# Performance work log

Measured on AMD Instinct MI355X. Metric: run time of the kernel, lower is better.

Reference implementation:

```python
import jax, jax.numpy as jnp
import numpy as np

EPS = 1e-5

def layer_norm(x, g, b):
    m = x.mean(-1, keepdims=True)
    v = ((x - m) ** 2).mean(-1, keepdims=True)
    return (x - m) * jax.lax.rsqrt(v + EPS) * g + b

def setup_inputs() -> dict:
    key = jax.random.key(0)
    ks = jax.random.split(key, 12)
    H = 2048; E = 2048; I = 2048; N = 32
    A = (H + E) // 2  # attention hidden = 2048
    s = lambda fan: 1.0 / np.sqrt(fan)
    inp = {
        "input":   jax.random.normal(ks[0], (I,), jnp.float32),
        "hiddens": jax.random.normal(ks[1], (N, H), jnp.float32),
        "cells":   jax.random.normal(ks[2], (N, H), jnp.float32),
        "external":jax.random.normal(ks[3], (E,), jnp.float32),
        # weights (torch nn.Linear layout: [out, in]); LN enabled -> no biases on linears
        "W_ai":   jax.random.uniform(ks[4], (A, H + E), jnp.float32, -s(H+E), s(H+E)),
        "W_attn": jax.random.uniform(ks[5], (1, A), jnp.float32, -s(A), s(A)),
        "W_merge":jax.random.uniform(ks[6], (H, H), jnp.float32, -s(H), s(H)),
        "W_iou":  jax.random.uniform(ks[7], (3 * H, I + H), jnp.float32, -s(I+H), s(I+H)),
        "W_fi":   jax.random.uniform(ks[8], (H, I), jnp.float32, -s(I), s(I)),
        "W_fh":   jax.random.uniform(ks[9], (H, H), jnp.float32, -s(H), s(H)),
        "g_merge": jnp.ones((H,), jnp.float32), "b_merge": jnp.zeros((H,), jnp.float32),
        "g_f": jnp.ones((H,), jnp.float32), "b_f": jnp.zeros((H,), jnp.float32),
        "g_i": jnp.ones((H,), jnp.float32), "b_i": jnp.zeros((H,), jnp.float32),
        "g_o": jnp.ones((H,), jnp.float32), "b_o": jnp.zeros((H,), jnp.float32),
        "g_u": jnp.ones((H,), jnp.float32), "b_u": jnp.zeros((H,), jnp.float32),
        "g_c": jnp.ones((H,), jnp.float32), "b_c": jnp.zeros((H,), jnp.float32),
    }
    return inp

def reference(input, hiddens, cells, external,
              W_ai, W_attn, W_merge, W_iou, W_fi, W_fh,
              g_merge, b_merge, g_f, b_f, g_i, b_i, g_o, b_o, g_u, b_u, g_c, b_c):
    N, H = hiddens.shape
    # forget-gate preactivations: [H] + [N,H] -> [N,H]
    f_lin = input @ W_fi.T + hiddens @ W_fh.T
    # attentive merge over children
    ext = jnp.broadcast_to(external, (N, external.shape[0]))
    ai = jnp.tanh(jnp.concatenate([hiddens, ext], axis=1) @ W_ai.T)       # [N, (H+E)//2]
    attn = jax.nn.softmax(ai @ W_attn.T, axis=0)                          # [N, 1]
    merged = (hiddens * attn).sum(0)                                      # [H]
    merge_hidden = jnp.tanh(layer_norm(merged @ W_merge.T, g_merge, b_merge))
    # i/o/u gates from [input ; merged_hidden]
    iou = jnp.concatenate([input, merge_hidden]) @ W_iou.T                # [3H]
    i_l, o_l, u_l = jnp.split(iou, 3)
    f = jax.nn.sigmoid(layer_norm(f_lin, g_f, b_f))                       # [N,H]
    i = jax.nn.sigmoid(layer_norm(i_l, g_i, b_i))
    o = jax.nn.sigmoid(layer_norm(o_l, g_o, b_o))
    u = jnp.tanh(layer_norm(u_l, g_u, b_u))                               # dropout=0 -> identity
    new_cell = layer_norm(i * u + (f * cells).sum(0), g_c, b_c)           # [H]
    new_h = o * jnp.tanh(new_cell)
    return new_h, new_cell
```

## Files before the change

### kernel.cpp

```cpp
#include <hip/hip_runtime.h>
#include <hip/hip_bf16.h>

typedef __bf16 bf16_t;
typedef __attribute__((ext_vector_type(8))) __bf16 bf16x8;
typedef __attribute__((ext_vector_type(4))) float f32x4;

#define EPSF 1e-5f

__global__ __launch_bounds__(256) void gemm32_mfma(
    const float* __restrict__ Hd, const float* __restrict__ W,
    float* __restrict__ C, int M, int K, int wstride, int jtiles)
{
    int bx   = blockIdx.x;
    int jt   = bx % jtiles;
    int nt   = bx / jtiles;
    int tid  = threadIdx.x;
    int wave = tid >> 6;
    int lane = tid & 63;
    int l15  = lane & 15;
    int quad = lane >> 4;
    int kper = K >> 2;
    int k0   = wave * kper;

    const float* ap = Hd + (size_t)(nt * 16 + l15) * 2048 + quad * 8 + k0;
    const float* bp = W  + (size_t)(jt * 16 + l15) * wstride + quad * 8 + k0;

    f32x4 acc = {0.f, 0.f, 0.f, 0.f};
    for (int k = 0; k < kper; k += 32) {
        float4 a0 = *(const float4*)(ap + k);
        float4 a1 = *(const float4*)(ap + k + 4);
        float4 b0 = *(const float4*)(bp + k);
        float4 b1 = *(const float4*)(bp + k + 4);
        bf16x8 av, bv;
        av[0] = (bf16_t)a0.x; av[1] = (bf16_t)a0.y; av[2] = (bf16_t)a0.z; av[3] = (bf16_t)a0.w;
        av[4] = (bf16_t)a1.x; av[5] = (bf16_t)a1.y; av[6] = (bf16_t)a1.z; av[7] = (bf16_t)a1.w;
        bv[0] = (bf16_t)b0.x; bv[1] = (bf16_t)b0.y; bv[2] = (bf16_t)b0.z; bv[3] = (bf16_t)b0.w;
        bv[4] = (bf16_t)b1.x; bv[5] = (bf16_t)b1.y; bv[6] = (bf16_t)b1.z; bv[7] = (bf16_t)b1.w;
        acc = __builtin_amdgcn_mfma_f32_16x16x32_bf16(av, bv, acc, 0, 0, 0);
    }

    __shared__ float red[4][16][16];
    #pragma unroll
    for (int r = 0; r < 4; ++r) red[wave][quad * 4 + r][l15] = acc[r];
    __syncthreads();

    int row = tid >> 4, col = tid & 15;
    float s = red[0][row][col] + red[1][row][col] + red[2][row][col] + red[3][row][col];
    C[(size_t)(nt * 16 + row) * M + jt * 16 + col] = s;
}

__global__ __launch_bounds__(256) void gemv_k(
    const float* __restrict__ W, const float* __restrict__ x,
    float* __restrict__ out, int K, int wstride)
{
    int row  = blockIdx.x * 4 + (threadIdx.x >> 6);
    int lane = threadIdx.x & 63;
    const float4* wp = (const float4*)(W + (size_t)row * wstride) + lane;
    const float4* xp = (const float4*)x + lane;
    int kq = K >> 2;
    float acc = 0.f;
    for (int k = 0; k < kq; k += 64) {
        float4 w = wp[k];
        float4 v = xp[k];
        acc += w.x * v.x + w.y * v.y + w.z * v.z + w.w * v.w;
    }
    #pragma unroll
    for (int off = 32; off; off >>= 1) acc += __shfl_down(acc, off, 64);
    if (lane == 0) out[row] = acc;
}

__global__ __launch_bounds__(256) void attn_part(
    const float* __restrict__ ai, const float* __restrict__ ej,
    const float* __restrict__ wattn, float* __restrict__ lp)
{
    int b    = blockIdx.x;
    int wave = threadIdx.x >> 6;
    int lane = threadIdx.x & 63;
    int j    = b * 64 + lane;
    float e  = ej[j];
    float wa = wattn[j];
    #pragma unroll
    for (int i = 0; i < 8; ++i) {
        int n = wave * 8 + i;
        float v = tanhf(ai[n * 2048 + j] + e) * wa;
        #pragma unroll
        for (int off = 32; off; off >>= 1) v += __shfl_down(v, off, 64);
        if (lane == 0) lp[b * 32 + n] = v;
    }
}

__global__ __launch_bounds__(64) void attn_fin(
    const float* __restrict__ lp, float* __restrict__ attn)
{
    int lane = threadIdx.x;
    float logit = -1e30f;
    if (lane < 32) {
        float s = 0.f;
        for (int b = 0; b < 32; ++b) s += lp[b * 32 + lane];
        logit = s;
    }
    float m = logit;
    #pragma unroll
    for (int off = 32; off; off >>= 1) m = fmaxf(m, __shfl_xor(m, off, 64));
    float e = (lane < 32) ? expf(logit - m) : 0.f;
    float s = e;
    #pragma unroll
    for (int off = 32; off; off >>= 1) s += __shfl_xor(s, off, 64);
    if (lane < 32) attn[lane] = e / s;
}

__global__ __launch_bounds__(256) void merge_k(
    const float* __restrict__ attn, const float* __restrict__ hiddens,
    float* __restrict__ merged)
{
    int h = blockIdx.x * 256 + threadIdx.x;
    float acc = 0.f;
    #pragma unroll 8
    for (int n = 0; n < 32; ++n) acc += attn[n] * hiddens[n * 2048 + h];
    merged[h] = acc;
}

__global__ __launch_bounds__(256) void ln_cat(
    const float* __restrict__ mm, const float* __restrict__ g, const float* __restrict__ b,
    const float* __restrict__ input, float* __restrict__ xcat)
{
    __shared__ float s1[256], s2[256];
    int t = threadIdx.x;
    float v[8]; float sum = 0.f, sq = 0.f;
    #pragma unroll
    for (int i = 0; i < 8; ++i) {
        v[i] = mm[t * 8 + i]; sum += v[i]; sq += v[i] * v[i];
    }
    s1[t] = sum; s2[t] = sq;
    __syncthreads();
    for (int off = 128; off; off >>= 1) {
        if (t < off) { s1[t] += s1[t + off]; s2[t] += s2[t + off]; }
        __syncthreads();
    }
    const float inv = 1.f / 2048.f;
    float mean = s1[0] * inv;
    float r = rsqrtf(s2[0] * inv - mean * mean + EPSF);
    #pragma unroll
    for (int i = 0; i < 8; ++i) {
        int h = t * 8 + i;
        xcat[2048 + h] = tanhf((v[i] - mean) * r * g[h] + b[h]);
        xcat[h] = input[h];
    }
}

__global__ __launch_bounds__(256) void f_stats(
    const float* __restrict__ fi, const float* __restrict__ fh, float* __restrict__ frs)
{
    __shared__ float s1[256], s2[256];
    int n = blockIdx.x, t = threadIdx.x;
    float sum = 0.f, sq = 0.f;
    #pragma unroll
    for (int i = 0; i < 8; ++i) {
        int h = t * 8 + i;
        float v = fi[h] + fh[n * 2048 + h];
        sum += v; sq += v * v;
    }
    s1[t] = sum; s2[t] = sq;
    __syncthreads();
    for (int off = 128; off; off >>= 1) {
        if (t < off) { s1[t] += s1[t + off]; s2[t] += s2[t + off]; }
        __syncthreads();
    }
    if (t == 0) {
        const float inv = 1.f / 2048.f;
        float mean = s1[0] * inv;
        float var  = s2[0] * inv - mean * mean;
        frs[n * 2]     = mean;
        frs[n * 2 + 1] = rsqrtf(var + EPSF);
    }
}

__global__ __launch_bounds__(256) void fc_sum(
    const float* __restrict__ fi, const float* __restrict__ fh, const float* __restrict__ frs,
    const float* __restrict__ gf, const float* __restrict__ bf_,
    const float* __restrict__ cells, float* __restrict__ fc)
{
    int h = blockIdx.x * 256 + threadIdx.x;
    float g = gf[h], bb = bf_[h], f_i = fi[h];
    float acc = 0.f;
    for (int n = 0; n < 32; ++n) {
        float v = (f_i + fh[n * 2048 + h] - frs[n * 2]) * frs[n * 2 + 1] * g + bb;
        float f = 1.f / (1.f + expf(-v));
        acc += f * cells[n * 2048 + h];
    }
    fc[h] = acc;
}

__global__ __launch_bounds__(256) void tail_k(
    const float* __restrict__ iou, const float* __restrict__ fc,
    const float* __restrict__ gi, const float* __restrict__ bi,
    const float* __restrict__ go, const float* __restrict__ bo,
    const float* __restrict__ gu, const float* __restrict__ bu,
    const float* __restrict__ gc, const float* __restrict__ bc,
    float* __restrict__ out)
{
    __shared__ float sA[6][256];
    int t = threadIdx.x;
    float vi[8], vo[8], vu[8];
    float si = 0, qi = 0, so = 0, qo = 0, su = 0, qu = 0;
    #pragma unroll
    for (int i = 0; i < 8; ++i) {
        int h = t * 8 + i;
        vi[i] = iou[h]; vo[i] = iou[2048 + h]; vu[i] = iou[4096 + h];
        si += vi[i]; qi += vi[i] * vi[i];
        so += vo[i]; qo += vo[i] * vo[i];
        su += vu[i]; qu += vu[i] * vu[i];
    }
    sA[0][t] = si; sA[1][t] = qi; sA[2][t] = so;
    sA[3][t] = qo; sA[4][t] = su; sA[5][t] = qu;
    __syncthreads();
    for (int off = 128; off; off >>= 1) {
        if (t < off) {
            #pragma unroll
            for (int c = 0; c < 6; ++c) sA[c][t] += sA[c][t + off];
        }
        __syncthreads();
    }
    const float inv = 1.f / 2048.f;
    float mi = sA[0][0] * inv, ri = rsqrtf(sA[1][0] * inv - mi * mi + EPSF);
    float mo = sA[2][0] * inv, ro = rsqrtf(sA[3][0] * inv - mo * mo + EPSF);
    float mu = sA[4][0] * inv, ru = rsqrtf(sA[5][0] * inv - mu * mu + EPSF);
    __syncthreads();

    float o_[8], v_[8];
    float sv = 0, qv = 0;
    #pragma unroll
    for (int i = 0; i < 8; ++i) {
        int h = t * 8 + i;
        float ivl = 1.f / (1.f + expf(-((vi[i] - mi) * ri * gi[h] + bi[h])));
        o_[i]     = 1.f / (1.f + expf(-((vo[i] - mo) * ro * go[h] + bo[h])));
        float uvl = tanhf((vu[i] - mu) * ru * gu[h] + bu[h]);
        v_[i] = ivl * uvl + fc[h];
        sv += v_[i]; qv += v_[i] * v_[i];
    }
    sA[0][t] = sv; sA[1][t] = qv;
    __syncthreads();
    for (int off = 128; off; off >>= 1) {
        if (t < off) { sA[0][t] += sA[0][t + off]; sA[1][t] += sA[1][t + off]; }
        __syncthreads();
    }
    float mc = sA[0][0] * inv, rc = rsqrtf(sA[1][0] * inv - mc * mc + EPSF);
    #pragma unroll
    for (int i = 0; i < 8; ++i) {
        int h = t * 8 + i;
        float nc = (v_[i] - mc) * rc * gc[h] + bc[h];
        float nh = o_[i] * tanhf(nc);
        out[h]        = nh;
        out[2048 + h] = nc;
    }
}

extern "C" void kernel_launch(void* const* d_in, const int* in_sizes, int n_in,
                              void* d_out, int out_size, void* d_ws, size_t ws_size,
                              hipStream_t stream)
{
    const float* input    = (const float*)d_in[0];
    const float* hiddens  = (const float*)d_in[1];
    const float* cells    = (const float*)d_in[2];
    const float* external = (const float*)d_in[3];
    const float* W_ai     = (const float*)d_in[4];
    const float* W_attn   = (const float*)d_in[5];
    const float* W_merge  = (const float*)d_in[6];
    const float* W_iou    = (const float*)d_in[7];
    const float* W_fi     = (const float*)d_in[8];
    const float* W_fh     = (const float*)d_in[9];
    const float* g_merge  = (const float*)d_in[10];
    const float* b_merge  = (const float*)d_in[11];
    const float* g_f      = (const float*)d_in[12];
    const float* b_f      = (const float*)d_in[13];
    const float* g_i      = (const float*)d_in[14];
    const float* b_i      = (const float*)d_in[15];
    const float* g_o      = (const float*)d_in[16];
    const float* b_o      = (const float*)d_in[17];
    const float* g_u      = (const float*)d_in[18];
    const float* b_u      = (const float*)d_in[19];
    const float* g_c      = (const float*)d_in[20];
    const float* b_c      = (const float*)d_in[21];

    float* ws = (float*)d_ws;
    float* ws_ai     = ws;
    float* ws_fh     = ws + 65536;
    float* ws_ej     = ws + 131072;
    float* ws_fi     = ws + 133120;
    float* ws_lp     = ws + 135168;
    float* ws_attn   = ws + 136192;
    float* ws_mm     = ws + 136224;
    float* ws_fc     = ws + 138272;
    float* ws_iou    = ws + 140320;
    float* ws_frs    = ws + 146464;
    float* ws_merged = ws + 146528;
    float* ws_xcat   = ws + 148576;
    float* out = (float*)d_out;

    gemm32_mfma<<<256, 256, 0, stream>>>(hiddens, W_ai, ws_ai, 2048, 2048, 4096, 128);
    gemm32_mfma<<<256, 256, 0, stream>>>(hiddens, W_fh, ws_fh, 2048, 2048, 2048, 128);
    gemv_k<<<512, 256, 0, stream>>>(W_ai + 2048, external, ws_ej, 2048, 4096);
    gemv_k<<<512, 256, 0, stream>>>(W_fi, input, ws_fi, 2048, 2048);

    attn_part<<<32, 256, 0, stream>>>(ws_ai, ws_ej, W_attn, ws_lp);
    attn_fin<<<1, 64, 0, stream>>>(ws_lp, ws_attn);
    merge_k<<<8, 256, 0, stream>>>(ws_attn, hiddens, ws_merged);
    gemv_k<<<512, 256, 0, stream>>>(W_merge, ws_merged, ws_mm, 2048, 2048);
    ln_cat<<<1, 256, 0, stream>>>(ws_mm, g_merge, b_merge, input, ws_xcat);
    gemv_k<<<1536, 256, 0, stream>>>(W_iou, ws_xcat, ws_iou, 4096, 4096);

    f_stats<<<32, 256, 0, stream>>>(ws_fi, ws_fh, ws_frs);
    fc_sum<<<8, 256, 0, stream>>>(ws_fi, ws_fh, ws_frs, g_f, b_f, cells, ws_fc);

    tail_k<<<1, 256, 0, stream>>>(ws_iou, ws_fc, g_i, b_i, g_o, b_o,
                                  g_u, b_u, g_c, b_c, out);
}
```

Before: 313.6 us.

## Fuse thirteen launches into five staged mega-kernels with fused attention epilogue

Merges the two MFMA GEMMs and the two GEMVs into one launch, computing the external projection inside the W_ai GEMM loop and applying tanh·W_attn in its epilogue so the [32,2048] ai matrix is never written. Softmax and the attention-weighted merge are fused with the forget-gate stats, the merge GEMV with fc_sum, and the merge LayerNorm is recomputed per block inside the iou GEMV. This removes launch overheads and intermediate round-trips, at the cost of 384 blocks redundantly computing the LayerNorm and a larger inner loop in the ai blocks.

```diff
diff --git a/kernel.cpp b/kernel.cpp
--- a/kernel.cpp
+++ b/kernel.cpp
@@ -7,125 +7,222 @@
 
 #define EPSF 1e-5f
 
-__global__ __launch_bounds__(256) void gemm32_mfma(
-    const float* __restrict__ Hd, const float* __restrict__ W,
-    float* __restrict__ C, int M, int K, int wstride, int jtiles)
-{
-    int bx   = blockIdx.x;
-    int jt   = bx % jtiles;
-    int nt   = bx / jtiles;
+__global__ __launch_bounds__(256) void s1_mega(
+    const float* __restrict__ hiddens, const float* __restrict__ external,
+    const float* __restrict__ input,
+    const float* __restrict__ W_ai, const float* __restrict__ W_fh,
+    const float* __restrict__ W_fi, const float* __restrict__ W_attn,
+    float* __restrict__ lp, float* __restrict__ fh_out, float* __restrict__ fi_out)
+{
+    __shared__ float red[4][16][16];
+    __shared__ float ejs[4][16];
+
+    int b    = blockIdx.x;
     int tid  = threadIdx.x;
     int wave = tid >> 6;
     int lane = tid & 63;
-    int l15  = lane & 15;
-    int quad = lane >> 4;
-    int kper = K >> 2;
-    int k0   = wave * kper;
-
-    const float* ap = Hd + (size_t)(nt * 16 + l15) * 2048 + quad * 8 + k0;
-    const float* bp = W  + (size_t)(jt * 16 + l15) * wstride + quad * 8 + k0;
-
-    f32x4 acc = {0.f, 0.f, 0.f, 0.f};
-    for (int k = 0; k < kper; k += 32) {
-        float4 a0 = *(const float4*)(ap + k);
-        float4 a1 = *(const float4*)(ap + k + 4);
-        float4 b0 = *(const float4*)(bp + k);
-        float4 b1 = *(const float4*)(bp + k + 4);
-        bf16x8 av, bv;
-        av[0] = (bf16_t)a0.x; av[1] = (bf16_t)a0.y; av[2] = (bf16_t)a0.z; av[3] = (bf16_t)a0.w;
-        av[4] = (bf16_t)a1.x; av[5] = (bf16_t)a1.y; av[6] = (bf16_t)a1.z; av[7] = (bf16_t)a1.w;
-        bv[0] = (bf16_t)b0.x; bv[1] = (bf16_t)b0.y; bv[2] = (bf16_t)b0.z; bv[3] = (bf16_t)b0.w;
-        bv[4] = (bf16_t)b1.x; bv[5] = (bf16_t)b1.y; bv[6] = (bf16_t)b1.z; bv[7] = (bf16_t)b1.w;
-        acc = __builtin_amdgcn_mfma_f32_16x16x32_bf16(av, bv, acc, 0, 0, 0);
-    }
-
-    __shared__ float red[4][16][16];
-    #pragma unroll
-    for (int r = 0; r < 4; ++r) red[wave][quad * 4 + r][l15] = acc[r];
-    __syncthreads();
-
-    int row = tid >> 4, col = tid & 15;
-    float s = red[0][row][col] + red[1][row][col] + red[2][row][col] + red[3][row][col];
-    C[(size_t)(nt * 16 + row) * M + jt * 16 + col] = s;
-}
-
-__global__ __launch_bounds__(256) void gemv_k(
-    const float* __restrict__ W, const float* __restrict__ x,
-    float* __restrict__ out, int K, int wstride)
-{
-    int row  = blockIdx.x * 4 + (threadIdx.x >> 6);
-    int lane = threadIdx.x & 63;
-    const float4* wp = (const float4*)(W + (size_t)row * wstride) + lane;
-    const float4* xp = (const float4*)x + lane;
-    int kq = K >> 2;
-    float acc = 0.f;
-    for (int k = 0; k < kq; k += 64) {
-        float4 w = wp[k];
-        float4 v = xp[k];
-        acc += w.x * v.x + w.y * v.y + w.z * v.z + w.w * v.w;
-    }
-    #pragma unroll
-    for (int off = 32; off; off >>= 1) acc += __shfl_down(acc, off, 64);
-    if (lane == 0) out[row] = acc;
-}
-
-__global__ __launch_bounds__(256) void attn_part(
-    const float* __restrict__ ai, const float* __restrict__ ej,
-    const float* __restrict__ wattn, float* __restrict__ lp)
-{
-    int b    = blockIdx.x;
-    int wave = threadIdx.x >> 6;
-    int lane = threadIdx.x & 63;
-    int j    = b * 64 + lane;
-    float e  = ej[j];
-    float wa = wattn[j];
-    #pragma unroll
-    for (int i = 0; i < 8; ++i) {
-        int n = wave * 8 + i;
-        float v = tanhf(ai[n * 2048 + j] + e) * wa;
-        #pragma unroll
-        for (int off = 32; off; off >>= 1) v += __shfl_down(v, off, 64);
-        if (lane == 0) lp[b * 32 + n] = v;
-    }
-}
-
-__global__ __launch_bounds__(64) void attn_fin(
-    const float* __restrict__ lp, float* __restrict__ attn)
-{
-    int lane = threadIdx.x;
-    float logit = -1e30f;
-    if (lane < 32) {
-        float s = 0.f;
-        for (int b = 0; b < 32; ++b) s += lp[b * 32 + lane];
-        logit = s;
-    }
-    float m = logit;
-    #pragma unroll
-    for (int off = 32; off; off >>= 1) m = fmaxf(m, __shfl_xor(m, off, 64));
-    float e = (lane < 32) ? expf(logit - m) : 0.f;
-    float s = e;
-    #pragma unroll
-    for (int off = 32; off; off >>= 1) s += __shfl_xor(s, off, 64);
-    if (lane < 32) attn[lane] = e / s;
-}
-
-__global__ __launch_bounds__(256) void merge_k(
-    const float* __restrict__ attn, const float* __restrict__ hiddens,
-    float* __restrict__ merged)
-{
-    int h = blockIdx.x * 256 + threadIdx.x;
-    float acc = 0.f;
-    #pragma unroll 8
-    for (int n = 0; n < 32; ++n) acc += attn[n] * hiddens[n * 2048 + h];
-    merged[h] = acc;
-}
-
-__global__ __launch_bounds__(256) void ln_cat(
-    const float* __restrict__ mm, const float* __restrict__ g, const float* __restrict__ b,
-    const float* __restrict__ input, float* __restrict__ xcat)
+
+    if (b < 512) {
+        bool is_ai = (b < 256);
+        int  bb    = is_ai ? b : b - 256;
+        int  jt    = bb & 127;
+        int  nt    = bb >> 7;
+        int  l15   = lane & 15;
+        int  quad  = lane >> 4;
+        int  k0    = wave * 512;
+        int  wstride = is_ai ? 4096 : 2048;
+        const float* W = is_ai ? W_ai : W_fh;
+
+        const float* ap = hiddens + (size_t)(nt * 16 + l15) * 2048 + quad * 8 + k0;
+        const float* bp = W + (size_t)(jt * 16 + l15) * wstride + quad * 8 + k0;
+
+        f32x4 acc = {0.f, 0.f, 0.f, 0.f};
+        float ejacc = 0.f;
+
+        if (is_ai) {
+            const float* ep = bp + 2048;
+            const float* xp = external + quad * 8 + k0;
+            for (int k = 0; k < 512; k += 32) {
+                float4 a0 = *(const float4*)(ap + k);
+                float4 a1 = *(const float4*)(ap + k + 4);
+                float4 b0 = *(const float4*)(bp + k);
+                float4 b1 = *(const float4*)(bp + k + 4);
+                bf16x8 av, bv;
+                av[0]=(bf16_t)a0.x; av[1]=(bf16_t)a0.y; av[2]=(bf16_t)a0.z; av[3]=(bf16_t)a0.w;
+                av[4]=(bf16_t)a1.x; av[5]=(bf16_t)a1.y; av[6]=(bf16_t)a1.z; av[7]=(bf16_t)a1.w;
+                bv[0]=(bf16_t)b0.x; bv[1]=(bf16_t)b0.y; bv[2]=(bf16_t)b0.z; bv[3]=(bf16_t)b0.w;
+                bv[4]=(bf16_t)b1.x; bv[5]=(bf16_t)b1.y; bv[6]=(bf16_t)b1.z; bv[7]=(bf16_t)b1.w;
+                acc = __builtin_amdgcn_mfma_f32_16x16x32_bf16(av, bv, acc, 0, 0, 0);
+                float4 e0 = *(const float4*)(ep + k);
+                float4 e1 = *(const float4*)(ep + k + 4);
+                float4 x0 = *(const float4*)(xp + k);
+                float4 x1 = *(const float4*)(xp + k + 4);
+                ejacc += e0.x*x0.x + e0.y*x0.y + e0.z*x0.z + e0.w*x0.w
+                       + e1.x*x1.x + e1.y*x1.y + e1.z*x1.z + e1.w*x1.w;
+            }
+            ejacc += __shfl_xor(ejacc, 16, 64);
+            ejacc += __shfl_xor(ejacc, 32, 64);
+            if (quad == 0) ejs[wave][l15] = ejacc;
+        } else {
+            for (int k = 0; k < 512; k += 32) {
+                float4 a0 = *(const float4*)(ap + k);
+                float4 a1 = *(const float4*)(ap + k + 4);
+                float4 b0 = *(const float4*)(bp + k);
+                float4 b1 = *(const float4*)(bp + k + 4);
+                bf16x8 av, bv;
+                av[0]=(bf16_t)a0.x; av[1]=(bf16_t)a0.y; av[2]=(bf16_t)a0.z; av[3]=(bf16_t)a0.w;
+                av[4]=(bf16_t)a1.x; av[5]=(bf16_t)a1.y; av[6]=(bf16_t)a1.z; av[7]=(bf16_t)a1.w;
+                bv[0]=(bf16_t)b0.x; bv[1]=(bf16_t)b0.y; bv[2]=(bf16_t)b0.z; bv[3]=(bf16_t)b0.w;
+                bv[4]=(bf16_t)b1.x; bv[5]=(bf16_t)b1.y; bv[6]=(bf16_t)b1.z; bv[7]=(bf16_t)b1.w;
+                acc = __builtin_amdgcn_mfma_f32_16x16x32_bf16(av, bv, acc, 0, 0, 0);
+            }
+        }
+
+        #pragma unroll
+        for (int r = 0; r < 4; ++r) red[wave][quad * 4 + r][l15] = acc[r];
+        __syncthreads();
+
+        int row = tid >> 4, col = tid & 15;
+        float s = red[0][row][col] + red[1][row][col] + red[2][row][col] + red[3][row][col];
+
+        if (is_ai) {
+            float ej = ejs[0][col] + ejs[1][col] + ejs[2][col] + ejs[3][col];
+            float lg = tanhf(s + ej) * W_attn[jt * 16 + col];
+            lg += __shfl_xor(lg, 1, 64);
+            lg += __shfl_xor(lg, 2, 64);
+            lg += __shfl_xor(lg, 4, 64);
+            lg += __shfl_xor(lg, 8, 64);
+            if (col == 0) lp[jt * 32 + nt * 16 + row] = lg;
+        } else {
+            fh_out[(size_t)(nt * 16 + row) * 2048 + jt * 16 + col] = s;
+        }
+    } else {
+        int b2 = b - 512;
+        #pragma unroll
+        for (int r = 0; r < 4; ++r) {
+            int row = b2 * 16 + wave * 4 + r;
+            const float4* wp = (const float4*)(W_fi + (size_t)row * 2048) + lane;
+            const float4* xp = (const float4*)input + lane;
+            float acc2 = 0.f;
+            #pragma unroll
+            for (int k = 0; k < 512; k += 64) {
+                float4 w = wp[k];
+                float4 v = xp[k];
+                acc2 += w.x*v.x + w.y*v.y + w.z*v.z + w.w*v.w;
+            }
+            #pragma unroll
+            for (int off = 32; off; off >>= 1) acc2 += __shfl_down(acc2, off, 64);
+            if (lane == 0) fi_out[row] = acc2;
+        }
+    }
+}
+
+__global__ __launch_bounds__(256) void s2_mega(
+    const float* __restrict__ fi, const float* __restrict__ fh,
+    const float* __restrict__ lp, const float* __restrict__ hiddens,
+    float* __restrict__ frs, float* __restrict__ merged)
 {
     __shared__ float s1[256], s2[256];
-    int t = threadIdx.x;
+    int b = blockIdx.x, t = threadIdx.x;
+
+    if (b < 32) {
+        int n = b;
+        float sum = 0.f, sq = 0.f;
+        #pragma unroll
+        for (int i = 0; i < 8; ++i) {
+            int h = t * 8 + i;
+            float v = fi[h] + fh[n * 2048 + h];
+            sum += v; sq += v * v;
+        }
+        s1[t] = sum; s2[t] = sq;
+        __syncthreads();
+        for (int off = 128; off; off >>= 1) {
+            if (t < off) { s1[t] += s1[t + off]; s2[t] += s2[t + off]; }
+            __syncthreads();
+        }
+        if (t == 0) {
+            const float inv = 1.f / 2048.f;
+            float mean = s1[0] * inv;
+            frs[n * 2]     = mean;
+            frs[n * 2 + 1] = rsqrtf(s2[0] * inv - mean * mean + EPSF);
+        }
+    } else {
+        __shared__ float lred[32][8];
+        __shared__ float attnw[32];
+        int n = t >> 3, sl = t & 7;
+        float p = 0.f;
+        #pragma unroll
+        for (int m = 0; m < 16; ++m) p += lp[(sl * 16 + m) * 32 + n];
+        lred[n][sl] = p;
+        __syncthreads();
+        if (sl == 0) {
+            float lg = 0.f;
+            #pragma unroll
+            for (int m = 0; m < 8; ++m) lg += lred[n][m];
+            lred[n][0] = lg;
+        }
+        __syncthreads();
+        if (t < 32) {
+            float mx = -1e30f;
+            for (int m = 0; m < 32; ++m) mx = fmaxf(mx, lred[m][0]);
+            float ssum = 0.f;
+            for (int m = 0; m < 32; ++m) ssum += expf(lred[m][0] - mx);
+            attnw[t] = expf(lred[t][0] - mx) / ssum;
+        }
+        __syncthreads();
+        int h = (b - 32) * 256 + t;
+        float acc = 0.f;
+        #pragma unroll 8
+        for (int n2 = 0; n2 < 32; ++n2) acc += attnw[n2] * hiddens[n2 * 2048 + h];
+        merged[h] = acc;
+    }
+}
+
+__global__ __launch_bounds__(256) void s3_mega(
+    const float* __restrict__ W_merge, const float* __restrict__ merged,
+    const float* __restrict__ fi, const float* __restrict__ fh,
+    const float* __restrict__ frs, const float* __restrict__ gf,
+    const float* __restrict__ bf_, const float* __restrict__ cells,
+    float* __restrict__ mm, float* __restrict__ fc)
+{
+    int b = blockIdx.x, t = threadIdx.x;
+    if (b < 512) {
+        int row  = b * 4 + (t >> 6);
+        int lane = t & 63;
+        const float4* wp = (const float4*)(W_merge + (size_t)row * 2048) + lane;
+        const float4* xp = (const float4*)merged + lane;
+        float acc = 0.f;
+        #pragma unroll
+        for (int k = 0; k < 512; k += 64) {
+            float4 w = wp[k];
+            float4 v = xp[k];
+            acc += w.x*v.x + w.y*v.y + w.z*v.z + w.w*v.w;
+        }
+        #pragma unroll
+        for (int off = 32; off; off >>= 1) acc += __shfl_down(acc, off, 64);
+        if (lane == 0) mm[row] = acc;
+    } else {
+        int h = (b - 512) * 256 + t;
+        float g = gf[h], bb = bf_[h], f_i = fi[h];
+        float acc = 0.f;
+        for (int n = 0; n < 32; ++n) {
+            float v = (f_i + fh[n * 2048 + h] - frs[n * 2]) * frs[n * 2 + 1] * g + bb;
+            float f = 1.f / (1.f + expf(-v));
+            acc += f * cells[n * 2048 + h];
+        }
+        fc[h] = acc;
+    }
+}
+
+__global__ __launch_bounds__(256) void s4_iou(
+    const float* __restrict__ W_iou, const float* __restrict__ mm,
+    const float* __restrict__ input, const float* __restrict__ g,
+    const float* __restrict__ bvec, float* __restrict__ iou)
+{
+    __shared__ float xcat[4096];
+    __shared__ float s1[256], s2[256];
+    int b = blockIdx.x, t = threadIdx.x;
+
     float v[8]; float sum = 0.f, sq = 0.f;
     #pragma unroll
     for (int i = 0; i < 8; ++i) {
@@ -143,55 +240,31 @@
     #pragma unroll
     for (int i = 0; i < 8; ++i) {
         int h = t * 8 + i;
-        xcat[2048 + h] = tanhf((v[i] - mean) * r * g[h] + b[h]);
-        xcat[h] = input[h];
-    }
-}
-
-__global__ __launch_bounds__(256) void f_stats(
-    const float* __restrict__ fi, const float* __restrict__ fh, float* __restrict__ frs)
-{
-    __shared__ float s1[256], s2[256];
-    int n = blockIdx.x, t = threadIdx.x;
-    float sum = 0.f, sq = 0.f;
-    #pragma unroll
-    for (int i = 0; i < 8; ++i) {
-        int h = t * 8 + i;
-        float v = fi[h] + fh[n * 2048 + h];
-        sum += v; sq += v * v;
-    }
-    s1[t] = sum; s2[t] = sq;
-    __syncthreads();
-    for (int off = 128; off; off >>= 1) {
-        if (t < off) { s1[t] += s1[t + off]; s2[t] += s2[t + off]; }
-        __syncthreads();
-    }
-    if (t == 0) {
-        const float inv = 1.f / 2048.f;
-        float mean = s1[0] * inv;
-        float var  = s2[0] * inv - mean * mean;
-        frs[n * 2]     = mean;
-        frs[n * 2 + 1] = rsqrtf(var + EPSF);
-    }
-}
-
-__global__ __launch_bounds__(256) void fc_sum(
-    const float* __restrict__ fi, const float* __restrict__ fh, const float* __restrict__ frs,
-    const float* __restrict__ gf, const float* __restrict__ bf_,
-    const float* __restrict__ cells, float* __restrict__ fc)
-{
-    int h = blockIdx.x * 256 + threadIdx.x;
-    float g = gf[h], bb = bf_[h], f_i = fi[h];
-    float acc = 0.f;
-    for (int n = 0; n < 32; ++n) {
-        float v = (f_i + fh[n * 2048 + h] - frs[n * 2]) * frs[n * 2 + 1] * g + bb;
-        float f = 1.f / (1.f + expf(-v));
-        acc += f * cells[n * 2048 + h];
-    }
-    fc[h] = acc;
-}
-
-__global__ __launch_bounds__(256) void tail_k(
+        xcat[h]        = input[h];
+        xcat[2048 + h] = tanhf((v[i] - mean) * r * g[h] + bvec[h]);
+    }
+    __syncthreads();
+
+    int wave = t >> 6, lane = t & 63;
+    #pragma unroll
+    for (int rr = 0; rr < 4; ++rr) {
+        int row = b * 16 + wave * 4 + rr;
+        const float4* wp = (const float4*)(W_iou + (size_t)row * 4096) + lane;
+        const float4* xp = (const float4*)xcat + lane;
+        float acc = 0.f;
+        #pragma unroll
+        for (int k = 0; k < 1024; k += 64) {
+            float4 w = wp[k];
+            float4 x = xp[k];
+            acc += w.x*x.x + w.y*x.y + w.z*x.z + w.w*x.w;
+        }
+        #pragma unroll
+        for (int off = 32; off; off >>= 1) acc += __shfl_down(acc, off, 64);
+        if (lane == 0) iou[row] = acc;
+    }
+}
+
+__global__ __launch_bounds__(256) void s5_tail(
     const float* __restrict__ iou, const float* __restrict__ fc,
     const float* __restrict__ gi, const float* __restrict__ bi,
     const float* __restrict__ go, const float* __restrict__ bo,
@@ -283,35 +356,24 @@
     const float* b_c      = (const float*)d_in[21];
 
     float* ws = (float*)d_ws;
-    float* ws_ai     = ws;
-    float* ws_fh     = ws + 65536;
-    float* ws_ej     = ws + 131072;
-    float* ws_fi     = ws + 133120;
-    float* ws_lp     = ws + 135168;
-    float* ws_attn   = ws + 136192;
-    float* ws_mm     = ws + 136224;
-    float* ws_fc     = ws + 138272;
-    float* ws_iou    = ws + 140320;
-    float* ws_frs    = ws + 146464;
-    float* ws_merged = ws + 146528;
-    float* ws_xcat   = ws + 148576;
+    float* ws_fh     = ws;
+    float* ws_fi     = ws + 65536;
+    float* ws_lp     = ws + 67584;
+    float* ws_frs    = ws + 71680;
+    float* ws_merged = ws + 71744;
+    float* ws_mm     = ws + 73792;
+    float* ws_fc     = ws + 75840;
+    float* ws_iou    = ws + 77888;
     float* out = (float*)d_out;
 
-    gemm32_mfma<<<256, 256, 0, stream>>>(hiddens, W_ai, ws_ai, 2048, 2048, 4096, 128);
-    gemm32_mfma<<<256, 256, 0, stream>>>(hiddens, W_fh, ws_fh, 2048, 2048, 2048, 128);
-    gemv_k<<<512, 256, 0, stream>>>(W_ai + 2048, external, ws_ej, 2048, 4096);
-    gemv_k<<<512, 256, 0, stream>>>(W_fi, input, ws_fi, 2048, 2048);
-
-    attn_part<<<32, 256, 0, stream>>>(ws_ai, ws_ej, W_attn, ws_lp);
-    attn_fin<<<1, 64, 0, stream>>>(ws_lp, ws_attn);
-    merge_k<<<8, 256, 0, stream>>>(ws_attn, hiddens, ws_merged);
-    gemv_k<<<512, 256, 0, stream>>>(W_merge, ws_merged, ws_mm, 2048, 2048);
-    ln_cat<<<1, 256, 0, stream>>>(ws_mm, g_merge, b_merge, input, ws_xcat);
-    gemv_k<<<1536, 256, 0, stream>>>(W_iou, ws_xcat, ws_iou, 4096, 4096);
-
-    f_stats<<<32, 256, 0, stream>>>(ws_fi, ws_fh, ws_frs);
-    fc_sum<<<8, 256, 0, stream>>>(ws_fi, ws_fh, ws_frs, g_f, b_f, cells, ws_fc);
-
-    tail_k<<<1, 256, 0, stream>>>(ws_iou, ws_fc, g_i, b_i, g_o, b_o,
-                                  g_u, b_u, g_c, b_c, out);
-}
+    s1_mega<<<640, 256, 0, stream>>>(hiddens, external, input,
+                                     W_ai, W_fh, W_fi, W_attn,
+                                     ws_lp, ws_fh, ws_fi);
+    s2_mega<<<40, 256, 0, stream>>>(ws_fi, ws_fh, ws_lp, hiddens,
+                                    ws_frs, ws_merged);
+    s3_mega<<<520, 256, 0, stream>>>(W_merge, ws_merged, ws_fi, ws_fh,
+                                     ws_frs, g_f, b_f, cells, ws_mm, ws_fc);
+    s4_iou<<<384, 256, 0, stream>>>(W_iou, ws_mm, input, g_merge, b_merge, ws_iou);
+    s5_tail<<<1, 256, 0, stream>>>(ws_iou, ws_fc, g_i, b_i, g_o, b_o,
+                                   g_u, b_u, g_c, b_c, out);
+}
```

After: 279.7 us. 10.8% less time.
